# Optimization experiments

Hardware: AMD Instinct MI355X
Metric: run time of the kernel (lower is better)

Reference implementation:

```python
import jax, jax.numpy as jnp
import numpy as np

B, T, C = 2, 2048, 768
H, N_LEFT = 12, 6
D = C // H


def setup_inputs() -> dict:
    key = jax.random.key(0)
    ks = jax.random.split(key, 4)
    x = jax.random.normal(ks[0], (B, T, C), dtype=jnp.float32)
    attention_mask = jnp.ones((B, T), dtype=jnp.int32)
    Wqkv_w = jax.random.normal(ks[1], (3 * C, C), dtype=jnp.float32) * (C ** -0.5)
    Wqkv_b = jnp.zeros((3 * C,), dtype=jnp.float32)
    Wo_w = jax.random.normal(ks[2], (C, C), dtype=jnp.float32) * (C ** -0.5)
    Wo_b = jnp.zeros((C,), dtype=jnp.float32)
    return {"x": x, "attention_mask": attention_mask, "Wqkv_w": Wqkv_w,
            "Wqkv_b": Wqkv_b, "Wo_w": Wo_w, "Wo_b": Wo_b}


def _attend(q, k, v, mask):
    # q,k,v: [B,h,T,D]; mask: [B,1,T,T] additive
    s = jnp.einsum('bhqd,bhkd->bhqk', q, k) * (D ** -0.5) + mask
    a = jax.nn.softmax(s.astype(jnp.float32), axis=-1).astype(q.dtype)
    return jnp.einsum('bhqk,bhkd->bhqd', a, v)


def reference(x, attention_mask, Wqkv_w, Wqkv_b, Wo_w, Wo_b):
    neg = jnp.finfo(x.dtype).min
    # padding mask [B,1,1,T]: 0 where valid, neg where padded
    pad = (1.0 - attention_mask.astype(x.dtype))[:, None, None, :] * neg
    i = jnp.arange(T)
    tri = (i[None, :] > i[:, None]).astype(x.dtype) * neg   # triu(neg, 1)
    left_mask = tri[None, None] + pad                        # causal (look left)
    right_mask = tri.T[None, None] + pad                     # anti-causal (look right)

    qkv = (x @ Wqkv_w.T + Wqkv_b).reshape(B, T, 3, H, D)
    qkv = jnp.transpose(qkv, (0, 3, 2, 1, 4))                # [B,H,3,T,D]
    q, k, v = qkv[:, :, 0], qkv[:, :, 1], qkv[:, :, 2]

    lc = _attend(q[:, :N_LEFT], k[:, :N_LEFT], v[:, :N_LEFT], left_mask)
    rc = _attend(q[:, N_LEFT:], k[:, N_LEFT:], v[:, N_LEFT:], right_mask)
    ctx = jnp.concatenate([lc, rc], axis=1)                  # [B,H,T,D]
    ctx = jnp.transpose(ctx, (0, 2, 1, 3)).reshape(B, T, C)
    out = ctx @ Wo_w.T + Wo_b
    return out
```

## Files before the change

### kernel.cpp

```cpp
#include <hip/hip_runtime.h>


typedef unsigned short u16;
typedef __bf16 bf16x8 __attribute__((ext_vector_type(8)));
typedef float fx4 __attribute__((ext_vector_type(4)));
typedef unsigned short u16x8 __attribute__((ext_vector_type(8)));
typedef unsigned short u16x4 __attribute__((ext_vector_type(4)));
typedef _Float16 hx4 __attribute__((ext_vector_type(4)));
typedef __fp16 fp16x2 __attribute__((ext_vector_type(2)));

#define T_SEQ 2048
#define C_DIM 768
#define NHEAD 12
#define HDIM  64
#define NITEMS 768
#define LOG2E_8 0.18033688f

__device__ __forceinline__ u16 f2bf(float f) {
  unsigned u = __float_as_uint(f);
  u += 0x7fffu + ((u >> 16) & 1u);
  return (u16)(u >> 16);
}
__device__ __forceinline__ u16 f2h(float f) {
  union { _Float16 h; u16 u; } cv; cv.h = (_Float16)f; return cv.u;
}

__device__ __forceinline__ void gl2lds16(const u16* g, u16* l) {
  __builtin_amdgcn_global_load_lds(
      (const __attribute__((address_space(1))) void*)g,
      (__attribute__((address_space(3))) void*)l, 16, 0, 0);
}

__global__ void cvt_swz_k(const float* __restrict__ x,
                          const float* __restrict__ wqkv,
                          const float* __restrict__ wo,
                          u16* __restrict__ out) {
  int i = blockIdx.x * blockDim.x + threadIdx.x;
  if (i >= 688128) return;
  int m = i / 96;
  int c8 = (i - m * 96) << 3;
  const float* src;
  if (m < 4096)       src = x    + (size_t)m * C_DIM + c8;
  else if (m < 6400)  src = wqkv + (size_t)(m - 4096) * C_DIM + c8;
  else                src = wo   + (size_t)(m - 6400) * C_DIM + c8;
  fx4 a = *(const fx4*)src, b = *(const fx4*)(src + 4);
  u16x8 o;
  #pragma unroll
  for (int j = 0; j < 4; ++j) { o[j] = f2bf(a[j]); o[4 + j] = f2bf(b[j]); }
  *(u16x8*)&out[(size_t)m * C_DIM + (c8 ^ ((m & 7) << 3))] = o;
}

__global__ void maskcvt_k(const int* __restrict__ am, float* __restrict__ mf, int n) {
  int i = blockIdx.x * blockDim.x + threadIdx.x;
  if (i < n) mf[i] = am[i] ? 0.f : -1e30f;
}

__device__ __forceinline__ void gemm_core_64x128(const u16* __restrict__ A,
                                                 const u16* __restrict__ B,
                                                 int m0, int n0,
                                                 u16* As, u16* Bs,
                                                 fx4 acc[4][2]) {
  const int tid = threadIdx.x;
  const int lane = tid & 63, wv = tid >> 6;
  const int wn = wv << 5;
  const int lr = lane & 15, lg = lane >> 4;
  const int swk = (lr & 7) << 3;
  const int scol = (tid & 7) << 3;
  #pragma unroll
  for (int mt = 0; mt < 4; ++mt)
    #pragma unroll
    for (int nt = 0; nt < 2; ++nt) acc[mt][nt] = fx4{0.f, 0.f, 0.f, 0.f};

  #pragma unroll
  for (int p = 0; p < 2; ++p) {
    int row = (tid >> 3) + (p << 5);
    gl2lds16(&A[(size_t)(m0 + row) * C_DIM + scol], &As[(row << 6) + scol]);
  }
  #pragma unroll
  for (int p = 0; p < 4; ++p) {
    int row = (tid >> 3) + (p << 5);
    gl2lds16(&B[(size_t)(n0 + row) * C_DIM + scol], &Bs[(row << 6) + scol]);
  }

  int buf = 0;
  for (int k0 = 0; k0 < C_DIM; k0 += 64, buf ^= 1) {
    __syncthreads();
    if (k0 + 64 < C_DIM) {
      u16* Ad = &As[(buf ^ 1) << 12];
      u16* Bd = &Bs[(buf ^ 1) << 13];
      #pragma unroll
      for (int p = 0; p < 2; ++p) {
        int row = (tid >> 3) + (p << 5);
        gl2lds16(&A[(size_t)(m0 + row) * C_DIM + k0 + 64 + scol], &Ad[(row << 6) + scol]);
      }
      #pragma unroll
      for (int p = 0; p < 4; ++p) {
        int row = (tid >> 3) + (p << 5);
        gl2lds16(&B[(size_t)(n0 + row) * C_DIM + k0 + 64 + scol], &Bd[(row << 6) + scol]);
      }
    }
    const u16* Ab = &As[buf << 12];
    const u16* Bb = &Bs[buf << 13];
    #pragma unroll
    for (int kk = 0; kk < 64; kk += 32) {
      bf16x8 af[4], bfr[2];
      #pragma unroll
      for (int mt = 0; mt < 4; ++mt)
        af[mt] = *(const bf16x8*)&Ab[((mt * 16 + lr) << 6) + ((kk + lg * 8) ^ swk)];
      #pragma unroll
      for (int nt = 0; nt < 2; ++nt)
        bfr[nt] = *(const bf16x8*)&Bb[((wn + nt * 16 + lr) << 6) + ((kk + lg * 8) ^ swk)];
      #pragma unroll
      for (int mt = 0; mt < 4; ++mt)
        #pragma unroll
        for (int nt = 0; nt < 2; ++nt)
          acc[mt][nt] = __builtin_amdgcn_mfma_f32_16x16x32_bf16(
              af[mt], bfr[nt], acc[mt][nt], 0, 0, 0);
    }
  }
}

__global__ __launch_bounds__(256) void gemm_qkv_k(
    const u16* __restrict__ A, const u16* __restrict__ B,
    const float* __restrict__ bias,
    u16* __restrict__ qb, u16* __restrict__ kswz, u16* __restrict__ vswz) {
  __shared__ __align__(16) u16 As[2][64 * 64];
  __shared__ __align__(16) u16 Bs[2][128 * 64];
  int m0 = blockIdx.y << 6, n0 = blockIdx.x << 7;
  fx4 acc[4][2];
  gemm_core_64x128(A, B, m0, n0, &As[0][0], &Bs[0][0], acc);

  const int tid = threadIdx.x, lane = tid & 63, wv = tid >> 6;
  const int wn = wv << 5;
  const int lr = lane & 15, lg = lane >> 4;
  const int part = n0 / 768;

  if (part < 2) {
    #pragma unroll
    for (int nt = 0; nt < 2; ++nt) {
      int n = n0 + wn + nt * 16 + lr;
      float bv = bias[n];
      int rem = n - part * 768;
      int h = rem >> 6, d = rem & 63;
      #pragma unroll
      for (int mt = 0; mt < 4; ++mt) {
        #pragma unroll
        for (int r = 0; r < 4; ++r) {
          int m = m0 + mt * 16 + lg * 4 + r;
          int bb = m >> 11, t = m & 2047;
          int bh = bb * NHEAD + h;
          int kt = t >> 6, tr = t & 63;
          float val = acc[mt][nt][r] + bv;
          if (part == 0)
            qb[(((size_t)bh << 11) + t) * HDIM + d] = f2bf(val);
          else
            kswz[((size_t)(bh * 32 + kt) << 12) + (tr << 6) + (d ^ ((tr & 7) << 3))] =
                f2bf(val);
        }
      }
    }
  } else {
    u16* Vs = &Bs[0][0];
    __syncthreads();
    #pragma unroll
    for (int nt = 0; nt < 2; ++nt) {
      int n_local = wn + nt * 16 + lr;
      float bv = bias[n0 + n_local];
      #pragma unroll
      for (int mt = 0; mt < 4; ++mt) {
        u16x4 pk;
        #pragma unroll
        for (int r = 0; r < 4; ++r) pk[r] = f2h(acc[mt][nt][r] + bv);
        int m4 = (mt << 2) + lg;
        *(u16x4*)&Vs[(n_local << 6) + ((m4 ^ (n_local & 15)) << 2)] = pk;
      }
    }
    __syncthreads();
    int bb = m0 >> 11, kt = (m0 >> 6) & 31;
    int tr4 = tid & 15;
    #pragma unroll
    for (int p = 0; p < 8; ++p) {
      int n_local = (tid >> 4) + (p << 4);
      int nglob = n0 - 1536 + n_local;
      int h = nglob >> 6, d = nglob & 63;
      u16x4 v = *(const u16x4*)&Vs[(n_local << 6) + ((tr4 ^ (n_local & 15)) << 2)];
      size_t tile = (size_t)((bb * NHEAD + h) * 32 + kt) << 12;
      *(u16x4*)&vswz[tile + (d << 6) + ((tr4 ^ (d & 15)) << 2)] = v;
    }
  }
}

__device__ __forceinline__ void gemm_core_64x64(const u16* __restrict__ A,
                                                const u16* __restrict__ B,
                                                int m0, int n0,
                                                u16* As, u16* Bs,
                                                fx4 acc[2][2]) {
  const int tid = threadIdx.x;
  const int lane = tid & 63, wv = tid >> 6;
  const int wm = (wv & 1) << 5, wn = (wv >> 1) << 5;
  const int lr = lane & 15, lg = lane >> 4;
  const int swk = (lr & 7) << 3;
  const int scol = (tid & 7) << 3;
  #pragma unroll
  for (int mt = 0; mt < 2; ++mt)
    #pragma unroll
    for (int nt = 0; nt < 2; ++nt) acc[mt][nt] = fx4{0.f, 0.f, 0.f, 0.f};

  #pragma unroll
  for (int p = 0; p < 2; ++p) {
    int row = (tid >> 3) + (p << 5);
    gl2lds16(&A[(size_t)(m0 + row) * C_DIM + scol], &As[(row << 6) + scol]);
    gl2lds16(&B[(size_t)(n0 + row) * C_DIM + scol], &Bs[(row << 6) + scol]);
  }

  int buf = 0;
  for (int k0 = 0; k0 < C_DIM; k0 += 64, buf ^= 1) {
    __syncthreads();
    if (k0 + 64 < C_DIM) {
      u16* Ad = &As[(buf ^ 1) << 12];
      u16* Bd = &Bs[(buf ^ 1) << 12];
      #pragma unroll
      for (int p = 0; p < 2; ++p) {
        int row = (tid >> 3) + (p << 5);
        gl2lds16(&A[(size_t)(m0 + row) * C_DIM + k0 + 64 + scol], &Ad[(row << 6) + scol]);
        gl2lds16(&B[(size_t)(n0 + row) * C_DIM + k0 + 64 + scol], &Bd[(row << 6) + scol]);
      }
    }
    const u16* Ab = &As[buf << 12];
    const u16* Bb = &Bs[buf << 12];
    #pragma unroll
    for (int kk = 0; kk < 64; kk += 32) {
      bf16x8 af[2], bfr[2];
      #pragma unroll
      for (int mt = 0; mt < 2; ++mt)
        af[mt] = *(const bf16x8*)&Ab[((wm + mt * 16 + lr) << 6) + ((kk + lg * 8) ^ swk)];
      #pragma unroll
      for (int nt = 0; nt < 2; ++nt)
        bfr[nt] = *(const bf16x8*)&Bb[((wn + nt * 16 + lr) << 6) + ((kk + lg * 8) ^ swk)];
      #pragma unroll
      for (int mt = 0; mt < 2; ++mt)
        #pragma unroll
        for (int nt = 0; nt < 2; ++nt)
          acc[mt][nt] = __builtin_amdgcn_mfma_f32_16x16x32_bf16(
              af[mt], bfr[nt], acc[mt][nt], 0, 0, 0);
    }
  }
}

__global__ __launch_bounds__(256) void gemm_out_k(
    const u16* __restrict__ A, const u16* __restrict__ B,
    const float* __restrict__ bias, float* __restrict__ out) {
  __shared__ __align__(16) u16 As[2][64 * 64];
  __shared__ __align__(16) u16 Bs[2][64 * 64];
  int m0 = blockIdx.y << 6, n0 = blockIdx.x << 6;
  fx4 acc[2][2];
  gemm_core_64x64(A, B, m0, n0, &As[0][0], &Bs[0][0], acc);

  const int tid = threadIdx.x, lane = tid & 63, wv = tid >> 6;
  const int wm = (wv & 1) << 5, wn = (wv >> 1) << 5;
  const int lr = lane & 15, lg = lane >> 4;
  #pragma unroll
  for (int nt = 0; nt < 2; ++nt) {
    int n = n0 + wn + nt * 16 + lr;
    float bv = bias[n];
    #pragma unroll
    for (int mt = 0; mt < 2; ++mt) {
      #pragma unroll
      for (int r = 0; r < 4; ++r) {
        int m = m0 + wm + mt * 16 + lg * 4 + r;
        out[(size_t)m * C_DIM + n] = acc[mt][nt][r] + bv;
      }
    }
  }
}

__global__ __launch_bounds__(256) void attn_k(
    const u16* __restrict__ q, const u16* __restrict__ kswz,
    const u16* __restrict__ vswz, const float* __restrict__ maskf,
    u16* __restrict__ ctx, int* __restrict__ counter) {
  __shared__ __align__(16) u16 Ks[2][4096];
  __shared__ __align__(16) u16 Vt[2][4096];
  __shared__ int s_w;

  const int tid = threadIdx.x, lane = tid & 63, wv = tid >> 6;
  const int lr = lane & 15, lg = lane >> 4;
  const int swk = (lr & 7) << 3;
  const int swv = (lr & 15) << 2;

  for (;;) {
    if (tid == 0) s_w = atomicAdd(counter, 1);
    __syncthreads();
    int w = s_w;
    if (w >= NITEMS) break;
    int qslot = w / 24, bh = w - qslot * 24;
    int bb = bh / NHEAD, h = bh - bb * NHEAD;
    bool causal = (h < 6);
    int qt = causal ? (31 - qslot) : qslot;
    int kt0 = causal ? 0 : qt;
    int kt1 = causal ? qt : 31;
    size_t tile_base = (size_t)(bh * 32) << 12;

    {
      const u16* kg = kswz + tile_base + ((size_t)kt0 << 12);
      const u16* vg = vswz + tile_base + ((size_t)kt0 << 12);
      #pragma unroll
      for (int c2 = 0; c2 < 2; ++c2) {
        int e = (wv << 10) + (c2 << 9) + (lane << 3);
        gl2lds16(kg + e, &Ks[0][e]);
        gl2lds16(vg + e, &Vt[0][e]);
      }
    }

    int q0 = qt << 6;
    size_t head_off = ((size_t)bh << 11) * HDIM;
    int qrow = q0 + wv * 16 + lr;
    bf16x8 qf0 = *(const bf16x8*)&q[head_off + (size_t)qrow * HDIM + lg * 8];
    bf16x8 qf1 = *(const bf16x8*)&q[head_off + (size_t)qrow * HDIM + 32 + lg * 8];
    const float* mrow = maskf + (bb << 11);

    fx4 o[4];
    #pragma unroll
    for (int dt = 0; dt < 4; ++dt) o[dt] = fx4{0.f, 0.f, 0.f, 0.f};
    float l_i = 0.f;

    int buf = 0;
    for (int kt = kt0; kt <= kt1; ++kt, buf ^= 1) {
      __syncthreads();
      if (kt < kt1) {
        const u16* kg = kswz + tile_base + ((size_t)(kt + 1) << 12);
        const u16* vg = vswz + tile_base + ((size_t)(kt + 1) << 12);
        #pragma unroll
        for (int c2 = 0; c2 < 2; ++c2) {
          int e = (wv << 10) + (c2 << 9) + (lane << 3);
          gl2lds16(kg + e, &Ks[buf ^ 1][e]);
          gl2lds16(vg + e, &Vt[buf ^ 1][e]);
        }
      }

      fx4 st[4];
      #pragma unroll
      for (int nt = 0; nt < 4; ++nt) {
        const u16* kr = &Ks[buf][(nt * 16 + lr) << 6];
        bf16x8 kf0 = *(const bf16x8*)&kr[(lg * 8) ^ swk];
        bf16x8 kf1 = *(const bf16x8*)&kr[(32 + lg * 8) ^ swk];
        fx4 z = fx4{0.f, 0.f, 0.f, 0.f};
        z = __builtin_amdgcn_mfma_f32_16x16x32_bf16(kf0, qf0, z, 0, 0, 0);
        st[nt] = __builtin_amdgcn_mfma_f32_16x16x32_bf16(kf1, qf1, z, 0, 0, 0);
      }

      float psum = 0.f;
      if (kt == qt) {
        #pragma unroll
        for (int nt = 0; nt < 4; ++nt) {
          int kb0 = (kt << 6) + nt * 16 + lg * 4;
          fx4 mv = *(const fx4*)&mrow[kb0];
          #pragma unroll
          for (int r = 0; r < 4; ++r) {
            float arg = st[nt][r] * LOG2E_8 + mv[r];
            int kabs = kb0 + r;
            bool dead = causal ? (kabs > qrow) : (kabs < qrow);
            arg = dead ? -1e30f : arg;
            float p = __builtin_amdgcn_exp2f(arg);
            st[nt][r] = p;
            psum += p;
          }
        }
      } else {
        #pragma unroll
        for (int nt = 0; nt < 4; ++nt) {
          int kb0 = (kt << 6) + nt * 16 + lg * 4;
          fx4 mv = *(const fx4*)&mrow[kb0];
          #pragma unroll
          for (int r = 0; r < 4; ++r) {
            float p = __builtin_amdgcn_exp2f(st[nt][r] * LOG2E_8 + mv[r]);
            st[nt][r] = p;
            psum += p;
          }
        }
      }
      l_i += psum;

      #pragma unroll
      for (int nt = 0; nt < 4; ++nt) {
        union { hx4 v; fp16x2 h[2]; } pu;
        pu.h[0] = __builtin_amdgcn_cvt_pkrtz(st[nt][0], st[nt][1]);
        pu.h[1] = __builtin_amdgcn_cvt_pkrtz(st[nt][2], st[nt][3]);
        hx4 pf = pu.v;
        #pragma unroll
        for (int dt = 0; dt < 4; ++dt) {
          const u16* vr = &Vt[buf][(dt * 16 + lr) << 6];
          hx4 vf = *(const hx4*)&vr[(nt * 16 + lg * 4) ^ swv];
          o[dt] = __builtin_amdgcn_mfma_f32_16x16x16f16(vf, pf, o[dt], 0, 0, 0);
        }
      }
    }

    l_i += __shfl_xor(l_i, 16, 64);
    l_i += __shfl_xor(l_i, 32, 64);
    float inv = 1.f / l_i;
    size_t rowb = ((size_t)(bb << 11) + qrow) * C_DIM;
    int csw = (qrow & 7) << 3;
    #pragma unroll
    for (int dt = 0; dt < 4; ++dt) {
      u16x4 pk;
      #pragma unroll
      for (int r = 0; r < 4; ++r) pk[r] = f2bf(o[dt][r] * inv);
      int colb = h * HDIM + dt * 16 + lg * 4;
      *(u16x4*)&ctx[rowb + (colb ^ csw)] = pk;
    }
  }
}

extern "C" void kernel_launch(void* const* d_in, const int* in_sizes, int n_in,
                              void* d_out, int out_size, void* d_ws, size_t ws_size,
                              hipStream_t stream) {
  const float* x     = (const float*)d_in[0];
  const int*   amask = (const int*)d_in[1];
  const float* wqkv  = (const float*)d_in[2];
  const float* bqkv  = (const float*)d_in[3];
  const float* wo    = (const float*)d_in[4];
  const float* bo    = (const float*)d_in[5];
  float* out = (float*)d_out;

  char* ws = (char*)d_ws;
  u16*   xb    = (u16*)(ws + 0);
  u16*   wqkvb = (u16*)(ws + 6291456);
  u16*   wob   = (u16*)(ws + 9830400);
  u16*   qb    = (u16*)(ws + 11010048);
  u16*   kswz  = (u16*)(ws + 17301504);
  u16*   vswz  = (u16*)(ws + 23592960);
  u16*   ctxb  = (u16*)(ws + 29884416);
  float* maskf = (float*)(ws + 36175872);
  int*   cnt   = (int*)(ws + 36192256);

  cvt_swz_k<<<2688, 256, 0, stream>>>(x, wqkv, wo, xb);
  maskcvt_k<<<16, 256, 0, stream>>>(amask, maskf, 4096);
  (void)hipMemsetAsync(cnt, 0, 4, stream);

  gemm_qkv_k<<<dim3(18, 64), 256, 0, stream>>>(xb, wqkvb, bqkv, qb, kswz, vswz);
  attn_k<<<512, 256, 0, stream>>>(qb, kswz, vswz, maskf, ctxb, cnt);
  gemm_out_k<<<dim3(12, 64), 256, 0, stream>>>(ctxb, wob, bo, out);
}
```

Measured before the change: 174.2 us.

## Stage Q/K epilogue through LDS, skip mask loads for unpadded tiles, fold memset

The Q/K epilogue of the QKV GEMM now stages results in shared memory and writes 4-element vectors to global memory, replacing scattered 2-byte stores. The mask kernel also computes per-batch bitmasks that flag which 64-key tiles contain padding, so attention skips loading the mask for tiles with none. The counter reset moves into the mask kernel, which removes a separate memset launch. The costs are an extra barrier in every GEMM block and a small per-tile branch.

```diff
diff --git a/kernel.cpp b/kernel.cpp
--- a/kernel.cpp
+++ b/kernel.cpp
@@ -50,9 +50,23 @@
   *(u16x8*)&out[(size_t)m * C_DIM + (c8 ^ ((m & 7) << 3))] = o;
 }
 
-__global__ void maskcvt_k(const int* __restrict__ am, float* __restrict__ mf, int n) {
+__global__ void maskcvt_k(const int* __restrict__ am, float* __restrict__ mf,
+                          unsigned* __restrict__ fbits, int* __restrict__ cnt) {
   int i = blockIdx.x * blockDim.x + threadIdx.x;
-  if (i < n) mf[i] = am[i] ? 0.f : -1e30f;
+  if (i < 4096) mf[i] = am[i] ? 0.f : -1e30f;
+  if (blockIdx.x == 16) {
+    int t = threadIdx.x;
+    if (t == 0) cnt[0] = 0;
+    if (t < 64) {
+      int bb = t >> 5, kt = t & 31;
+      const int* seg = am + (bb << 11) + (kt << 6);
+      int anyz = 0;
+      for (int j = 0; j < 64; ++j) anyz |= (seg[j] == 0);
+      unsigned long long bal = __ballot(anyz != 0);
+      if (t == 0)  fbits[0] = (unsigned)(bal & 0xffffffffull);
+      if (t == 32) fbits[1] = (unsigned)(bal >> 32);
+    }
+  }
 }
 
 __device__ __forceinline__ void gemm_core_64x128(const u16* __restrict__ A,
@@ -134,56 +148,64 @@
   const int wn = wv << 5;
   const int lr = lane & 15, lg = lane >> 4;
   const int part = n0 / 768;
+  const int n0r = n0 - part * 768;
+  const int bb = m0 >> 11, kt = (m0 >> 6) & 31;
+  u16* Sc = &Bs[0][0];
+  __syncthreads();
 
   if (part < 2) {
     #pragma unroll
     for (int nt = 0; nt < 2; ++nt) {
-      int n = n0 + wn + nt * 16 + lr;
-      float bv = bias[n];
-      int rem = n - part * 768;
-      int h = rem >> 6, d = rem & 63;
+      int nl = wn + nt * 16 + lr;
+      float bv = bias[n0 + nl];
       #pragma unroll
       for (int mt = 0; mt < 4; ++mt) {
         #pragma unroll
         for (int r = 0; r < 4; ++r) {
-          int m = m0 + mt * 16 + lg * 4 + r;
-          int bb = m >> 11, t = m & 2047;
-          int bh = bb * NHEAD + h;
-          int kt = t >> 6, tr = t & 63;
-          float val = acc[mt][nt][r] + bv;
-          if (part == 0)
-            qb[(((size_t)bh << 11) + t) * HDIM + d] = f2bf(val);
-          else
-            kswz[((size_t)(bh * 32 + kt) << 12) + (tr << 6) + (d ^ ((tr & 7) << 3))] =
-                f2bf(val);
+          int m = mt * 16 + lg * 4 + r;
+          Sc[(m << 7) + (nl ^ ((m & 15) << 2))] = f2bf(acc[mt][nt][r] + bv);
         }
       }
     }
+    __syncthreads();
+    int c4 = (tid & 31) << 2;
+    int ng = n0r + c4;
+    int h = ng >> 6, d = ng & 63;
+    int bh = bb * NHEAD + h;
+    #pragma unroll
+    for (int p = 0; p < 8; ++p) {
+      int m = (tid >> 5) + (p << 3);
+      u16x4 v = *(const u16x4*)&Sc[(m << 7) + (c4 ^ ((m & 15) << 2))];
+      if (part == 0) {
+        int t = (m0 & 2047) + m;
+        *(u16x4*)&qb[(((size_t)bh << 11) + t) * HDIM + d] = v;
+      } else {
+        *(u16x4*)&kswz[((size_t)(bh * 32 + kt) << 12) + (m << 6) +
+                       (d ^ ((m & 7) << 3))] = v;
+      }
+    }
   } else {
-    u16* Vs = &Bs[0][0];
-    __syncthreads();
     #pragma unroll
     for (int nt = 0; nt < 2; ++nt) {
-      int n_local = wn + nt * 16 + lr;
-      float bv = bias[n0 + n_local];
+      int nl = wn + nt * 16 + lr;
+      float bv = bias[n0 + nl];
       #pragma unroll
       for (int mt = 0; mt < 4; ++mt) {
         u16x4 pk;
         #pragma unroll
         for (int r = 0; r < 4; ++r) pk[r] = f2h(acc[mt][nt][r] + bv);
         int m4 = (mt << 2) + lg;
-        *(u16x4*)&Vs[(n_local << 6) + ((m4 ^ (n_local & 15)) << 2)] = pk;
+        *(u16x4*)&Sc[(nl << 6) + ((m4 ^ (nl & 15)) << 2)] = pk;
       }
     }
     __syncthreads();
-    int bb = m0 >> 11, kt = (m0 >> 6) & 31;
     int tr4 = tid & 15;
     #pragma unroll
     for (int p = 0; p < 8; ++p) {
-      int n_local = (tid >> 4) + (p << 4);
-      int nglob = n0 - 1536 + n_local;
-      int h = nglob >> 6, d = nglob & 63;
-      u16x4 v = *(const u16x4*)&Vs[(n_local << 6) + ((tr4 ^ (n_local & 15)) << 2)];
+      int nl = (tid >> 4) + (p << 4);
+      int ng = n0r + nl;
+      int h = ng >> 6, d = ng & 63;
+      u16x4 v = *(const u16x4*)&Sc[(nl << 6) + ((tr4 ^ (nl & 15)) << 2)];
       size_t tile = (size_t)((bb * NHEAD + h) * 32 + kt) << 12;
       *(u16x4*)&vswz[tile + (d << 6) + ((tr4 ^ (d & 15)) << 2)] = v;
     }
@@ -277,6 +299,7 @@
 __global__ __launch_bounds__(256) void attn_k(
     const u16* __restrict__ q, const u16* __restrict__ kswz,
     const u16* __restrict__ vswz, const float* __restrict__ maskf,
+    const unsigned* __restrict__ fbits,
     u16* __restrict__ ctx, int* __restrict__ counter) {
   __shared__ __align__(16) u16 Ks[2][4096];
   __shared__ __align__(16) u16 Vt[2][4096];
@@ -299,6 +322,7 @@
     int kt0 = causal ? 0 : qt;
     int kt1 = causal ? qt : 31;
     size_t tile_base = (size_t)(bh * 32) << 12;
+    unsigned fb = fbits[bb];
 
     {
       const u16* kg = kswz + tile_base + ((size_t)kt0 << 12);
@@ -365,7 +389,7 @@
             psum += p;
           }
         }
-      } else {
+      } else if ((fb >> kt) & 1u) {
         #pragma unroll
         for (int nt = 0; nt < 4; ++nt) {
           int kb0 = (kt << 6) + nt * 16 + lg * 4;
@@ -377,6 +401,15 @@
             psum += p;
           }
         }
+      } else {
+        #pragma unroll
+        for (int nt = 0; nt < 4; ++nt)
+          #pragma unroll
+          for (int r = 0; r < 4; ++r) {
+            float p = __builtin_amdgcn_exp2f(st[nt][r] * LOG2E_8);
+            st[nt][r] = p;
+            psum += p;
+          }
       }
       l_i += psum;
 
@@ -423,21 +456,21 @@
   float* out = (float*)d_out;
 
   char* ws = (char*)d_ws;
-  u16*   xb    = (u16*)(ws + 0);
-  u16*   wqkvb = (u16*)(ws + 6291456);
-  u16*   wob   = (u16*)(ws + 9830400);
-  u16*   qb    = (u16*)(ws + 11010048);
-  u16*   kswz  = (u16*)(ws + 17301504);
-  u16*   vswz  = (u16*)(ws + 23592960);
-  u16*   ctxb  = (u16*)(ws + 29884416);
-  float* maskf = (float*)(ws + 36175872);
-  int*   cnt   = (int*)(ws + 36192256);
+  u16*      xb    = (u16*)(ws + 0);
+  u16*      wqkvb = (u16*)(ws + 6291456);
+  u16*      wob   = (u16*)(ws + 9830400);
+  u16*      qb    = (u16*)(ws + 11010048);
+  u16*      kswz  = (u16*)(ws + 17301504);
+  u16*      vswz  = (u16*)(ws + 23592960);
+  u16*      ctxb  = (u16*)(ws + 29884416);
+  float*    maskf = (float*)(ws + 36175872);
+  int*      cnt   = (int*)(ws + 36192256);
+  unsigned* fbits = (unsigned*)(ws + 36192320);
 
   cvt_swz_k<<<2688, 256, 0, stream>>>(x, wqkv, wo, xb);
-  maskcvt_k<<<16, 256, 0, stream>>>(amask, maskf, 4096);
-  (void)hipMemsetAsync(cnt, 0, 4, stream);
+  maskcvt_k<<<17, 256, 0, stream>>>(amask, maskf, fbits, cnt);
 
   gemm_qkv_k<<<dim3(18, 64), 256, 0, stream>>>(xb, wqkvb, bqkv, qb, kswz, vswz);
-  attn_k<<<512, 256, 0, stream>>>(qb, kswz, vswz, maskf, ctxb, cnt);
+  attn_k<<<512, 256, 0, stream>>>(qb, kswz, vswz, maskf, fbits, ctxb, cnt);
   gemm_out_k<<<dim3(12, 64), 256, 0, stream>>>(ctxb, wob, bo, out);
 }
```

After: 164.8 us. -5.4%, faster.
